# Kernel optimization log

Measured on AMD Instinct MI355X. Metric: run time of the kernel, lower is better.

Reference implementation:

```python
import jax, jax.numpy as jnp
import numpy as np

TEMPERATURE = 0.07
NEG = -1e9  # finite stand-in for -inf; exp(-1e9) underflows to 0 in fp32, identical math


def setup_inputs() -> dict:
    key = jax.random.key(0)
    k1, k2 = jax.random.split(key)
    B, D = 8192, 128
    emb = jax.random.normal(k1, (B, D), dtype=jnp.float32)
    emb = emb / jnp.linalg.norm(emb, axis=1, keepdims=True)  # docstring: normalized embeddings
    labels = jax.random.randint(k2, (B,), 0, 2048, dtype=jnp.int64)
    return {"embeddings": emb, "labels": labels}


def reference(embeddings, labels):
    B = labels.shape[0]
    # [B, B] pairwise similarities / temperature
    sim = jnp.matmul(embeddings, embeddings.T) / TEMPERATURE
    eye = jnp.eye(B, dtype=bool)
    sim = jnp.where(eye, NEG, sim)  # mask self-similarity
    # positives: same outfit id, excluding self
    pos_mask = (labels[None, :] == labels[:, None]) & (~eye)
    # row-wise log-softmax (torch code does log_softmax over each row)
    log_probs = jax.nn.log_softmax(sim, axis=1)
    pos_count = jnp.sum(pos_mask, axis=1)  # [B]
    pos_sum = jnp.sum(jnp.where(pos_mask, log_probs, 0.0), axis=1)  # [B]
    has_pos = pos_count > 0
    row_mean = jnp.where(has_pos, pos_sum / jnp.maximum(pos_count, 1), 0.0)
    count = jnp.sum(has_pos)
    loss = -jnp.sum(row_mean) / jnp.maximum(count, 1)
    return loss
```

## Files before the change

kernel.cpp:

```cpp
#include <hip/hip_runtime.h>


#define BATCH 8192
#define DIMK  128
#define INV_T 14.285714285714286f
#define MSUB  14.285714285714286f
#define K1    20.609929155311264f
#define K2    20.609929155311264f

typedef short bf16x8 __attribute__((ext_vector_type(8)));
typedef float f32x4  __attribute__((ext_vector_type(4)));

__device__ __forceinline__ unsigned short f2bf_rne(float f) {
    unsigned u = __float_as_uint(f);
    u += 0x7FFFu + ((u >> 16) & 1u);
    return (unsigned short)(u >> 16);
}
__device__ __forceinline__ float bf2f(unsigned short b) {
    return __uint_as_float(((unsigned)b) << 16);
}

__global__ __launch_bounds__(256) void
prep_kernel(const float* __restrict__ emb, const int* __restrict__ labels,
            ushort* __restrict__ Ebf, float* __restrict__ gsum, int* __restrict__ gcnt,
            float4* __restrict__ zzero) {
    if (blockIdx.x < 1024) {
        int i = blockIdx.x * 256 + threadIdx.x;
        if (i < 67584) {
            float4 z = {0.f, 0.f, 0.f, 0.f};
            zzero[i] = z;
        }
        float4 v = ((const float4*)emb)[i];
        ushort4 o;
        o.x = f2bf_rne(v.x); o.y = f2bf_rne(v.y);
        o.z = f2bf_rne(v.z); o.w = f2bf_rne(v.w);
        ((ushort4*)Ebf)[i] = o;
    } else {
        __shared__ int labs[BATCH];
        const int tid = threadIdx.x;
#pragma unroll
        for (int it = 0; it < 8; ++it)
            ((int4*)labs)[it * 256 + tid] = ((const int4*)labels)[it * 256 + tid];
        __syncthreads();

        const int lane = tid & 63;
        const int wid  = tid >> 6;
        const int c    = (blockIdx.x - 1024) * 4 + wid;
        float2 acc = {0.f, 0.f};
        int cnt = 0;
        int nl = labs[lane];
        for (int j0 = 0; j0 < BATCH; j0 += 64) {
            int cur = nl;
            int nidx = j0 + 64 < BATCH ? j0 + 64 : 0;
            nl = labs[nidx + lane];
            unsigned long long m = __ballot(cur == c);
            cnt += __popcll(m);
            while (m) {
                int j = __ffsll(m) - 1;
                m &= m - 1;
                float2 v = *(const float2*)(emb + (size_t)(j0 + j) * DIMK + lane * 2);
                acc.x += v.x; acc.y += v.y;
            }
        }
        *(float2*)(gsum + (size_t)c * DIMK + lane * 2) = acc;
        if (lane == 0) gcnt[c] = cnt;
    }
}

__global__ __launch_bounds__(256) void
contrastive_main(const ushort* __restrict__ Ebf, float* __restrict__ zpartR,
                 float* __restrict__ zcol) {
    __shared__ __align__(16) ushort Bs[2048 * 8];
    __shared__ float cpart[4][256];
    const int tid  = threadIdx.x;
    const int lane = tid & 63;
    const int wid  = tid >> 6;
    const int quad = lane >> 4;
    const int l16  = lane & 15;

    int b = blockIdx.x >> 1;
    const int half = blockIdx.x & 1;
    int ti = 0;
    while (b >= 32 - ti) { b -= 32 - ti; ++ti; }
    const int tj = ti + b;
    const int row_base = ti * 256 + half * 128 + wid * 32;

    bf16x8 afrag[2][4];
#pragma unroll
    for (int mt = 0; mt < 2; ++mt)
#pragma unroll
        for (int kk = 0; kk < 4; ++kk)
            afrag[mt][kk] = *(const bf16x8*)(Ebf + (size_t)(row_base + mt * 16 + l16) * DIMK
                                             + kk * 32 + quad * 8);

    float zacc[8];
#pragma unroll
    for (int s = 0; s < 8; ++s) zacc[s] = 0.f;

#pragma unroll
    for (int phase = 0; phase < 2; ++phase) {
        const int col_base = tj * 256 + phase * 128;
        __syncthreads();
#pragma unroll
        for (int it = 0; it < 8; ++it) {
            int f   = it * 256 + tid;
            int col = f >> 4;
            int c   = f & 15;
            uint4 v = *(const uint4*)(Ebf + (size_t)(col_base + col) * DIMK + c * 8);
            *(uint4*)&Bs[((col >> 4) * 256 + c * 16 + ((col & 15) ^ c)) * 8] = v;
        }
        __syncthreads();

        for (int nt = 0; nt < 8; ++nt) {
            bf16x8 bfrag[4];
#pragma unroll
            for (int kk = 0; kk < 4; ++kk) {
                const int c2 = kk * 4 + quad;
                bfrag[kk] = *(const bf16x8*)&Bs[(nt * 256 + c2 * 16 + (l16 ^ c2)) * 8];
            }

            float csum = 0.f;
#pragma unroll
            for (int mt = 0; mt < 2; ++mt) {
                f32x4 c = {0.f, 0.f, 0.f, 0.f};
#pragma unroll
                for (int kk = 0; kk < 4; ++kk)
                    c = __builtin_amdgcn_mfma_f32_16x16x32_bf16(afrag[mt][kk], bfrag[kk], c, 0, 0, 0);
#pragma unroll
                for (int r = 0; r < 4; ++r) {
                    float e = __builtin_amdgcn_exp2f(__builtin_fmaf(c[r], K1, -K2));
                    zacc[mt * 4 + r] += e;
                    csum += e;
                }
            }
            csum += __shfl_xor(csum, 16, 64);
            csum += __shfl_xor(csum, 32, 64);
            if (quad == 0) cpart[wid][phase * 128 + nt * 16 + l16] = csum;
        }
    }

#pragma unroll
    for (int s = 0; s < 8; ++s) {
        float z = zacc[s];
#pragma unroll
        for (int m = 1; m <= 8; m <<= 1) z += __shfl_xor(z, m, 64);
        if (l16 == 0) {
            int row = row_base + (s >> 2) * 16 + quad * 4 + (s & 3);
            zpartR[(size_t)tj * BATCH + row] = z;
        }
    }

    __syncthreads();
    if (ti != tj) {
        float s = cpart[0][tid] + cpart[1][tid] + cpart[2][tid] + cpart[3][tid];
        atomicAdd(&zcol[tj * 256 + tid], s);
    }
}

__global__ __launch_bounds__(256) void
finalize1(const float* __restrict__ emb, const ushort* __restrict__ Ebf,
          const int* __restrict__ labels, const float* __restrict__ gsum,
          const int* __restrict__ gcnt, const float* __restrict__ zpartR,
          const float* __restrict__ zcol,
          float* __restrict__ bpart, int* __restrict__ bcnt) {
    __shared__ float sf[4];
    __shared__ int   si[4];
    const int lane = threadIdx.x & 63;
    const int wid  = threadIdx.x >> 6;

    float wsum = 0.f;
    int   wcnt = 0;
#pragma unroll
    for (int it = 0; it < 4; ++it) {
        const int r   = blockIdx.x * 16 + wid * 4 + it;
        const int lab = labels[r];
        const int P   = gcnt[lab] - 1;

        float2 ev = *(const float2*)(emb  + (size_t)r   * DIMK + lane * 2);
        float2 gv = *(const float2*)(gsum + (size_t)lab * DIMK + lane * 2);
        unsigned bb = *(const unsigned*)(Ebf + (size_t)r * DIMK + lane * 2);
        float b0 = bf2f((unsigned short)(bb & 0xFFFF));
        float b1 = bf2f((unsigned short)(bb >> 16));

        float dotg = ev.x * gv.x + ev.y * gv.y;
        float ssd  = ev.x * ev.x + ev.y * ev.y;
        float sdbf = b0 * b0 + b1 * b1;
        float Z = 0.f;
        if (lane < 32)       Z = zpartR[(size_t)lane * BATCH + r];
        else if (lane == 32) Z = zcol[r];

#pragma unroll
        for (int m = 1; m <= 32; m <<= 1) {
            dotg += __shfl_xor(dotg, m, 64);
            ssd  += __shfl_xor(ssd,  m, 64);
            sdbf += __shfl_xor(sdbf, m, 64);
            Z    += __shfl_xor(Z,    m, 64);
        }
        Z -= __builtin_amdgcn_exp2f(__builtin_fmaf(sdbf, K1, -K2));

        const bool has = (P > 0);
        wsum += has ? ((dotg - ssd) * INV_T / (float)P - MSUB - __logf(Z)) : 0.f;
        wcnt += has ? 1 : 0;
    }

    if (lane == 0) { sf[wid] = wsum; si[wid] = wcnt; }
    __syncthreads();
    if (threadIdx.x == 0) {
        bpart[blockIdx.x] = sf[0] + sf[1] + sf[2] + sf[3];
        bcnt [blockIdx.x] = si[0] + si[1] + si[2] + si[3];
    }
}

__global__ __launch_bounds__(256) void
finalize2(const float* __restrict__ bpart, const int* __restrict__ bcnt,
          float* __restrict__ out) {
    __shared__ float sf[4];
    __shared__ int   si[4];
    const int t = threadIdx.x;
    float v = 0.f; int c = 0;
#pragma unroll
    for (int k = 0; k < 2; ++k) {
        v += bpart[t + k * 256];
        c += bcnt [t + k * 256];
    }
#pragma unroll
    for (int m = 1; m <= 32; m <<= 1) {
        v += __shfl_xor(v, m, 64);
        c += __shfl_xor(c, m, 64);
    }
    if ((t & 63) == 0) { sf[t >> 6] = v; si[t >> 6] = c; }
    __syncthreads();
    if (t == 0) {
        float tot = sf[0] + sf[1] + sf[2] + sf[3];
        int cc = si[0] + si[1] + si[2] + si[3];
        out[0] = -tot / (float)(cc > 0 ? cc : 1);
    }
}

extern "C" void kernel_launch(void* const* d_in, const int* in_sizes, int n_in,
                              void* d_out, int out_size, void* d_ws, size_t ws_size,
                              hipStream_t stream) {
    const float* emb  = (const float*)d_in[0];
    const int* labels = (const int*)d_in[1];
    float* out        = (float*)d_out;

    char* ws = (char*)d_ws;
    ushort* Ebf    = (ushort*)ws;
    float*  zpartR = (float*)(ws + (2u << 20));
    float*  zcol   = (float*)(ws + (3u << 20));
    float*  gsum   = (float*)(ws + (4u << 20));
    int*    gcnt   = (int*)  (ws + (5u << 20));
    float*  bpart  = (float*)(ws + (5u << 20) + 8192);
    int*    bcnt   = (int*)  (ws + (5u << 20) + 16384);

    prep_kernel<<<1536, 256, 0, stream>>>(emb, labels, Ebf, gsum, gcnt, (float4*)zpartR);
    contrastive_main<<<1056, 256, 0, stream>>>(Ebf, zpartR, zcol);
    finalize1<<<512, 256, 0, stream>>>(emb, Ebf, labels, gsum, gcnt, zpartR, zcol, bpart, bcnt);
    finalize2<<<1, 256, 0, stream>>>(bpart, bcnt, out);
}
```

Before: 101.4 us.

## Fuse prep into main kernel, convert fp32 to bf16 inline, drop atomics

Merges the bf16 conversion/group-sum prep kernel into the main similarity kernel: tiles now load fp32 embeddings and pack them to bf16 on the fly, while the extra blocks compute per-label sums. Column partial sums are written to a per-row-tile buffer instead of being accumulated with atomics, so the zeroing pass goes away. finalize1 reads only the valid triangular partials and recomputes the bf16 self-norm from fp32. This removes a kernel launch and the bf16 buffer round-trip, at the cost of twice the global load bytes per tile and conversion ALU work inside the main kernel.

After: 101.5 us. Within noise of the previous version (+0.2%).

```diff
diff --git a/kernel.cpp b/kernel.cpp
--- a/kernel.cpp
+++ b/kernel.cpp
@@ -19,33 +19,27 @@
 __device__ __forceinline__ float bf2f(unsigned short b) {
     return __uint_as_float(((unsigned)b) << 16);
 }
+__device__ __forceinline__ unsigned pk2(float a, float b) {
+    return (unsigned)f2bf_rne(a) | ((unsigned)f2bf_rne(b) << 16);
+}
 
 __global__ __launch_bounds__(256) void
-prep_kernel(const float* __restrict__ emb, const int* __restrict__ labels,
-            ushort* __restrict__ Ebf, float* __restrict__ gsum, int* __restrict__ gcnt,
-            float4* __restrict__ zzero) {
-    if (blockIdx.x < 1024) {
-        int i = blockIdx.x * 256 + threadIdx.x;
-        if (i < 67584) {
-            float4 z = {0.f, 0.f, 0.f, 0.f};
-            zzero[i] = z;
-        }
-        float4 v = ((const float4*)emb)[i];
-        ushort4 o;
-        o.x = f2bf_rne(v.x); o.y = f2bf_rne(v.y);
-        o.z = f2bf_rne(v.z); o.w = f2bf_rne(v.w);
-        ((ushort4*)Ebf)[i] = o;
-    } else {
-        __shared__ int labs[BATCH];
-        const int tid = threadIdx.x;
+fused_main(const float* __restrict__ emb, const int* __restrict__ labels,
+           float* __restrict__ zpartR, float* __restrict__ zpartC,
+           float* __restrict__ gsum, int* __restrict__ gcnt) {
+    __shared__ __align__(16) char smem[36864];
+    const int tid  = threadIdx.x;
+    const int lane = tid & 63;
+    const int wid  = tid >> 6;
+
+    if (blockIdx.x >= 1056) {
+        int* labs = (int*)smem;
 #pragma unroll
         for (int it = 0; it < 8; ++it)
             ((int4*)labs)[it * 256 + tid] = ((const int4*)labels)[it * 256 + tid];
         __syncthreads();
 
-        const int lane = tid & 63;
-        const int wid  = tid >> 6;
-        const int c    = (blockIdx.x - 1024) * 4 + wid;
+        const int c = (blockIdx.x - 1056) * 4 + wid;
         float2 acc = {0.f, 0.f};
         int cnt = 0;
         int nl = labs[lane];
@@ -64,17 +58,11 @@
         }
         *(float2*)(gsum + (size_t)c * DIMK + lane * 2) = acc;
         if (lane == 0) gcnt[c] = cnt;
-    }
-}
-
-__global__ __launch_bounds__(256) void
-contrastive_main(const ushort* __restrict__ Ebf, float* __restrict__ zpartR,
-                 float* __restrict__ zcol) {
-    __shared__ __align__(16) ushort Bs[2048 * 8];
-    __shared__ float cpart[4][256];
-    const int tid  = threadIdx.x;
-    const int lane = tid & 63;
-    const int wid  = tid >> 6;
+        return;
+    }
+
+    ushort* Bs = (ushort*)smem;
+    float (*cpart)[256] = (float(*)[256])(smem + 32768);
     const int quad = lane >> 4;
     const int l16  = lane & 15;
 
@@ -89,9 +77,15 @@
 #pragma unroll
     for (int mt = 0; mt < 2; ++mt)
 #pragma unroll
-        for (int kk = 0; kk < 4; ++kk)
-            afrag[mt][kk] = *(const bf16x8*)(Ebf + (size_t)(row_base + mt * 16 + l16) * DIMK
-                                             + kk * 32 + quad * 8);
+        for (int kk = 0; kk < 4; ++kk) {
+            const float* p = emb + (size_t)(row_base + mt * 16 + l16) * DIMK + kk * 32 + quad * 8;
+            float4 v0 = *(const float4*)p;
+            float4 v1 = *(const float4*)(p + 4);
+            union { bf16x8 h; uint4 u; } cv;
+            cv.u.x = pk2(v0.x, v0.y); cv.u.y = pk2(v0.z, v0.w);
+            cv.u.z = pk2(v1.x, v1.y); cv.u.w = pk2(v1.z, v1.w);
+            afrag[mt][kk] = cv.h;
+        }
 
     float zacc[8];
 #pragma unroll
@@ -106,8 +100,13 @@
             int f   = it * 256 + tid;
             int col = f >> 4;
             int c   = f & 15;
-            uint4 v = *(const uint4*)(Ebf + (size_t)(col_base + col) * DIMK + c * 8);
-            *(uint4*)&Bs[((col >> 4) * 256 + c * 16 + ((col & 15) ^ c)) * 8] = v;
+            const float* src = emb + (size_t)(col_base + col) * DIMK + c * 8;
+            float4 v0 = *(const float4*)src;
+            float4 v1 = *(const float4*)(src + 4);
+            uint4 w;
+            w.x = pk2(v0.x, v0.y); w.y = pk2(v0.z, v0.w);
+            w.z = pk2(v1.x, v1.y); w.w = pk2(v1.z, v1.w);
+            *(uint4*)&Bs[((col >> 4) * 256 + c * 16 + ((col & 15) ^ c)) * 8] = w;
         }
         __syncthreads();
 
@@ -153,15 +152,14 @@
     __syncthreads();
     if (ti != tj) {
         float s = cpart[0][tid] + cpart[1][tid] + cpart[2][tid] + cpart[3][tid];
-        atomicAdd(&zcol[tj * 256 + tid], s);
+        zpartC[(size_t)(ti * 2 + half) * BATCH + tj * 256 + tid] = s;
     }
 }
 
 __global__ __launch_bounds__(256) void
-finalize1(const float* __restrict__ emb, const ushort* __restrict__ Ebf,
-          const int* __restrict__ labels, const float* __restrict__ gsum,
-          const int* __restrict__ gcnt, const float* __restrict__ zpartR,
-          const float* __restrict__ zcol,
+finalize1(const float* __restrict__ emb, const int* __restrict__ labels,
+          const float* __restrict__ gsum, const int* __restrict__ gcnt,
+          const float* __restrict__ zpartR, const float* __restrict__ zpartC,
           float* __restrict__ bpart, int* __restrict__ bcnt) {
     __shared__ float sf[4];
     __shared__ int   si[4];
@@ -173,21 +171,26 @@
 #pragma unroll
     for (int it = 0; it < 4; ++it) {
         const int r   = blockIdx.x * 16 + wid * 4 + it;
+        const int tr  = r >> 8;
         const int lab = labels[r];
         const int P   = gcnt[lab] - 1;
 
         float2 ev = *(const float2*)(emb  + (size_t)r   * DIMK + lane * 2);
         float2 gv = *(const float2*)(gsum + (size_t)lab * DIMK + lane * 2);
-        unsigned bb = *(const unsigned*)(Ebf + (size_t)r * DIMK + lane * 2);
-        float b0 = bf2f((unsigned short)(bb & 0xFFFF));
-        float b1 = bf2f((unsigned short)(bb >> 16));
+        float b0 = bf2f(f2bf_rne(ev.x));
+        float b1 = bf2f(f2bf_rne(ev.y));
 
         float dotg = ev.x * gv.x + ev.y * gv.y;
         float ssd  = ev.x * ev.x + ev.y * ev.y;
         float sdbf = b0 * b0 + b1 * b1;
         float Z = 0.f;
-        if (lane < 32)       Z = zpartR[(size_t)lane * BATCH + r];
-        else if (lane == 32) Z = zcol[r];
+        if (lane < 32) {
+            if (lane >= tr) Z = zpartR[(size_t)lane * BATCH + r];
+        } else {
+            int s = lane - 32;
+            if (s < 2 * tr)      Z  = zpartC[(size_t)s * BATCH + r];
+            if (s + 32 < 2 * tr) Z += zpartC[(size_t)(s + 32) * BATCH + r];
+        }
 
 #pragma unroll
         for (int m = 1; m <= 32; m <<= 1) {
@@ -245,16 +248,14 @@
     float* out        = (float*)d_out;
 
     char* ws = (char*)d_ws;
-    ushort* Ebf    = (ushort*)ws;
-    float*  zpartR = (float*)(ws + (2u << 20));
-    float*  zcol   = (float*)(ws + (3u << 20));
-    float*  gsum   = (float*)(ws + (4u << 20));
-    int*    gcnt   = (int*)  (ws + (5u << 20));
-    float*  bpart  = (float*)(ws + (5u << 20) + 8192);
-    int*    bcnt   = (int*)  (ws + (5u << 20) + 16384);
-
-    prep_kernel<<<1536, 256, 0, stream>>>(emb, labels, Ebf, gsum, gcnt, (float4*)zpartR);
-    contrastive_main<<<1056, 256, 0, stream>>>(Ebf, zpartR, zcol);
-    finalize1<<<512, 256, 0, stream>>>(emb, Ebf, labels, gsum, gcnt, zpartR, zcol, bpart, bcnt);
+    float*  zpartR = (float*)ws;
+    float*  zpartC = (float*)(ws + (1u << 20));
+    float*  gsum   = (float*)(ws + (3u << 20));
+    int*    gcnt   = (int*)  (ws + (4u << 20));
+    float*  bpart  = (float*)(ws + (4u << 20) + 8192);
+    int*    bcnt   = (int*)  (ws + (4u << 20) + 16384);
+
+    fused_main<<<1568, 256, 0, stream>>>(emb, labels, zpartR, zpartC, gsum, gcnt);
+    finalize1<<<512, 256, 0, stream>>>(emb, labels, gsum, gcnt, zpartR, zpartC, bpart, bcnt);
     finalize2<<<1, 256, 0, stream>>>(bpart, bcnt, out);
 }
```

## Replace column atomics with per-tile partial buffers and shrink LDS staging

Applied to the files above, without the earlier changes.

The column-sum atomicAdds into zcol are replaced by plain stores into a per-row-tile partial buffer, which finalize1 then reduces, reading only the slots that were written. This removes the zero-initialisation pass in prep_kernel. The B-tile LDS staging is halved to 64 columns per phase over four phases with the inner loop fully unrolled, which should raise occupancy. finalize1 now recomputes the bf16 rounding from fp32 instead of reading Ebf. The cost is more __syncthreads per block and a larger workspace.

After: 102.8 us. No clear change (+1.4%).

```diff
diff --git a/kernel.cpp b/kernel.cpp
--- a/kernel.cpp
+++ b/kernel.cpp
@@ -22,14 +22,9 @@
 
 __global__ __launch_bounds__(256) void
 prep_kernel(const float* __restrict__ emb, const int* __restrict__ labels,
-            ushort* __restrict__ Ebf, float* __restrict__ gsum, int* __restrict__ gcnt,
-            float4* __restrict__ zzero) {
+            ushort* __restrict__ Ebf, float* __restrict__ gsum, int* __restrict__ gcnt) {
     if (blockIdx.x < 1024) {
         int i = blockIdx.x * 256 + threadIdx.x;
-        if (i < 67584) {
-            float4 z = {0.f, 0.f, 0.f, 0.f};
-            zzero[i] = z;
-        }
         float4 v = ((const float4*)emb)[i];
         ushort4 o;
         o.x = f2bf_rne(v.x); o.y = f2bf_rne(v.y);
@@ -69,8 +64,8 @@
 
 __global__ __launch_bounds__(256) void
 contrastive_main(const ushort* __restrict__ Ebf, float* __restrict__ zpartR,
-                 float* __restrict__ zcol) {
-    __shared__ __align__(16) ushort Bs[2048 * 8];
+                 float* __restrict__ zcolC) {
+    __shared__ __align__(16) ushort Bs[1024 * 8];
     __shared__ float cpart[4][256];
     const int tid  = threadIdx.x;
     const int lane = tid & 63;
@@ -98,11 +93,11 @@
     for (int s = 0; s < 8; ++s) zacc[s] = 0.f;
 
 #pragma unroll
-    for (int phase = 0; phase < 2; ++phase) {
-        const int col_base = tj * 256 + phase * 128;
+    for (int phase = 0; phase < 4; ++phase) {
+        const int col_base = tj * 256 + phase * 64;
         __syncthreads();
 #pragma unroll
-        for (int it = 0; it < 8; ++it) {
+        for (int it = 0; it < 4; ++it) {
             int f   = it * 256 + tid;
             int col = f >> 4;
             int c   = f & 15;
@@ -111,7 +106,8 @@
         }
         __syncthreads();
 
-        for (int nt = 0; nt < 8; ++nt) {
+#pragma unroll
+        for (int nt = 0; nt < 4; ++nt) {
             bf16x8 bfrag[4];
 #pragma unroll
             for (int kk = 0; kk < 4; ++kk) {
@@ -135,7 +131,7 @@
             }
             csum += __shfl_xor(csum, 16, 64);
             csum += __shfl_xor(csum, 32, 64);
-            if (quad == 0) cpart[wid][phase * 128 + nt * 16 + l16] = csum;
+            if (quad == 0) cpart[wid][phase * 64 + nt * 16 + l16] = csum;
         }
     }
 
@@ -153,15 +149,14 @@
     __syncthreads();
     if (ti != tj) {
         float s = cpart[0][tid] + cpart[1][tid] + cpart[2][tid] + cpart[3][tid];
-        atomicAdd(&zcol[tj * 256 + tid], s);
-    }
-}
-
-__global__ __launch_bounds__(256) void
-finalize1(const float* __restrict__ emb, const ushort* __restrict__ Ebf,
-          const int* __restrict__ labels, const float* __restrict__ gsum,
-          const int* __restrict__ gcnt, const float* __restrict__ zpartR,
-          const float* __restrict__ zcol,
+        zcolC[(size_t)(ti * 2 + half) * BATCH + tj * 256 + tid] = s;
+    }
+}
+
+__global__ __launch_bounds__(256) void
+finalize1(const float* __restrict__ emb, const int* __restrict__ labels,
+          const float* __restrict__ gsum, const int* __restrict__ gcnt,
+          const float* __restrict__ zpartR, const float* __restrict__ zpartC,
           float* __restrict__ bpart, int* __restrict__ bcnt) {
     __shared__ float sf[4];
     __shared__ int   si[4];
@@ -173,21 +168,26 @@
 #pragma unroll
     for (int it = 0; it < 4; ++it) {
         const int r   = blockIdx.x * 16 + wid * 4 + it;
+        const int tr  = r >> 8;
         const int lab = labels[r];
         const int P   = gcnt[lab] - 1;
 
         float2 ev = *(const float2*)(emb  + (size_t)r   * DIMK + lane * 2);
         float2 gv = *(const float2*)(gsum + (size_t)lab * DIMK + lane * 2);
-        unsigned bb = *(const unsigned*)(Ebf + (size_t)r * DIMK + lane * 2);
-        float b0 = bf2f((unsigned short)(bb & 0xFFFF));
-        float b1 = bf2f((unsigned short)(bb >> 16));
+        float b0 = bf2f(f2bf_rne(ev.x));
+        float b1 = bf2f(f2bf_rne(ev.y));
 
         float dotg = ev.x * gv.x + ev.y * gv.y;
         float ssd  = ev.x * ev.x + ev.y * ev.y;
         float sdbf = b0 * b0 + b1 * b1;
         float Z = 0.f;
-        if (lane < 32)       Z = zpartR[(size_t)lane * BATCH + r];
-        else if (lane == 32) Z = zcol[r];
+        if (lane < 32) {
+            if (lane >= tr) Z = zpartR[(size_t)lane * BATCH + r];
+        } else {
+            int s = lane - 32;
+            if (s < 2 * tr)      Z  = zpartC[(size_t)s * BATCH + r];
+            if (s + 32 < 2 * tr) Z += zpartC[(size_t)(s + 32) * BATCH + r];
+        }
 
 #pragma unroll
         for (int m = 1; m <= 32; m <<= 1) {
@@ -247,14 +247,14 @@
     char* ws = (char*)d_ws;
     ushort* Ebf    = (ushort*)ws;
     float*  zpartR = (float*)(ws + (2u << 20));
-    float*  zcol   = (float*)(ws + (3u << 20));
-    float*  gsum   = (float*)(ws + (4u << 20));
-    int*    gcnt   = (int*)  (ws + (5u << 20));
-    float*  bpart  = (float*)(ws + (5u << 20) + 8192);
-    int*    bcnt   = (int*)  (ws + (5u << 20) + 16384);
-
-    prep_kernel<<<1536, 256, 0, stream>>>(emb, labels, Ebf, gsum, gcnt, (float4*)zpartR);
-    contrastive_main<<<1056, 256, 0, stream>>>(Ebf, zpartR, zcol);
-    finalize1<<<512, 256, 0, stream>>>(emb, Ebf, labels, gsum, gcnt, zpartR, zcol, bpart, bcnt);
+    float*  zpartC = (float*)(ws + (3u << 20));
+    float*  gsum   = (float*)(ws + (5u << 20));
+    int*    gcnt   = (int*)  (ws + (6u << 20));
+    float*  bpart  = (float*)(ws + (6u << 20) + 8192);
+    int*    bcnt   = (int*)  (ws + (6u << 20) + 16384);
+
+    prep_kernel<<<1536, 256, 0, stream>>>(emb, labels, Ebf, gsum, gcnt);
+    contrastive_main<<<1056, 256, 0, stream>>>(Ebf, zpartR, zpartC);
+    finalize1<<<512, 256, 0, stream>>>(emb, labels, gsum, gcnt, zpartR, zpartC, bpart, bcnt);
     finalize2<<<1, 256, 0, stream>>>(bpart, bcnt, out);
 }
```
